# Optimization experiments

Hardware: AMD Instinct MI355X
Metric: run time of the kernel (lower is better)

Reference implementation:

```python
import jax, jax.numpy as jnp
import numpy as np

NUM_TASKS, IN_SIZE, OUT_SIZE, N_ROWS = 64, 512, 512, 2048


def setup_inputs() -> dict:
    key = jax.random.key(0)
    k_x, k_t, k_w = jax.random.split(key, 3)
    inputs = jax.random.normal(k_x, (N_ROWS, IN_SIZE), dtype=jnp.float32)
    task_ids = jax.random.randint(k_t, (N_ROWS,), 0, NUM_TASKS, dtype=jnp.int64)
    # in_size == out_size path: identity + N(0, 0.03) perturbation per task
    W = (jnp.eye(IN_SIZE, OUT_SIZE, dtype=jnp.float32)[None]
         + 0.03 * jax.random.normal(k_w, (NUM_TASKS, IN_SIZE, OUT_SIZE), dtype=jnp.float32))
    return {"inputs": inputs, "task_ids": task_ids, "W": W}


def reference(inputs, task_ids, W):
    # Gather the full per-row weight matrix then batched vector-matrix multiply,
    # faithful to torch.einsum('ni,nio->no', inputs, W[task_ids]).
    aligned = W[task_ids]                       # [I, in, out]
    return jnp.einsum("ni,nio->no", inputs, aligned)  # [I, out]
```

## Files before the change

kernel.cpp:

```cpp
#include <hip/hip_runtime.h>


#define NDIM 512
#define KDIM 512
#define NCOL 32
#define LISTCAP 256

typedef _Float16 f16x8 __attribute__((ext_vector_type(8)));
typedef float    f32x4 __attribute__((ext_vector_type(4)));
typedef int      i32x4 __attribute__((ext_vector_type(4)));

__global__ __launch_bounds__(256, 1) void k_wave(
    const float* __restrict__ x,
    const int*   __restrict__ tids,
    const float* __restrict__ W,
    float*       __restrict__ out,
    int n_rows)
{
    const int tid  = threadIdx.x;
    const int lane = tid & 63;
    const int wv   = tid >> 6;
    const int ml   = lane & 15;
    const int q    = lane >> 4;
    const int sc4  = (lane & 7) * 4;
    const int ol   = lane >> 3;

    const int bid   = blockIdx.x;
    const int task  = (bid & 7) | ((bid >> 5) << 3);
    const int chunk = ((bid >> 3) & 3) * 4 + wv;
    const int c0    = chunk * NCOL;

    __shared__ __align__(16) _Float16 Wt[4][NCOL * KDIM];
    __shared__ unsigned short rl[4][LISTCAP];

    _Float16*       Wm  = &Wt[wv][0];
    unsigned short* rlm = &rl[wv][0];

    const float* Wg = W + (size_t)task * KDIM * NDIM + c0;

    i32x4 tvv[8];
    #pragma unroll
    for (int cb = 0; cb < 8; ++cb) {
        const int r4 = cb * 256 + lane * 4;
        if (r4 + 3 < n_rows) {
            tvv[cb] = *(const i32x4*)(tids + r4);
        } else {
            #pragma unroll
            for (int j = 0; j < 4; ++j)
                tvv[cb][j] = (r4 + j < n_rows) ? tids[r4 + j] : -1;
        }
    }

    float4 wrA[8], wrB[8];
    auto issueS = [&](int s, float4 (&wb)[8]) {
        const size_t kb = (size_t)(ol + 8 * s) * 8;
        #pragma unroll
        for (int j = 0; j < 8; ++j)
            wb[j] = *(const float4*)(Wg + (kb + j) * NDIM + sc4);
    };
    auto stageS = [&](int s, const float4 (&wb)[8]) {
        const int oct = ol + 8 * s;
        #pragma unroll
        for (int j2 = 0; j2 < 4; ++j2) {
            f16x8 h8;
            #pragma unroll
            for (int j = 0; j < 8; ++j)
                h8[j] = (_Float16)(((const float*)&wb[j])[j2]);
            const int c  = sc4 + j2;
            const int po = oct ^ (c & 7);
            *(f16x8*)&Wm[c * KDIM + po * 8] = h8;
        }
    };

    issueS(0, wrA);
    issueS(1, wrB);

    int cnt = 0;
    #pragma unroll
    for (int cb = 0; cb < 8; ++cb) {
        #pragma unroll
        for (int j = 0; j < 4; ++j) {
            const bool m = (tvv[cb][j] == task);
            const unsigned long long bal = __ballot(m);
            const int rank = __popcll(bal & ((1ull << lane) - 1ull));
            const int slot = cnt + rank;
            if (m && slot < LISTCAP) rlm[slot] = (unsigned short)(cb * 256 + lane * 4 + j);
            cnt += __popcll(bal);
        }
    }
    if (cnt > LISTCAP) cnt = LISTCAP;

    stageS(0, wrA); issueS(2, wrA);
    stageS(1, wrB); issueS(3, wrB);
    stageS(2, wrA); issueS(4, wrA);
    stageS(3, wrB); issueS(5, wrB);
    stageS(4, wrA); issueS(6, wrA);
    stageS(5, wrB); issueS(7, wrB);
    stageS(6, wrA);
    stageS(7, wrB);

    f32x4 xqA[8], xqB[8];
    auto issueQ = [&](const float* xr, int qi, f32x4 (&xq)[8]) {
        #pragma unroll
        for (int s = 0; s < 4; ++s) {
            const int ks = qi * 4 + s;
            xq[2 * s]     = *(const f32x4*)(xr + ks * 32 + q * 8);
            xq[2 * s + 1] = *(const f32x4*)(xr + ks * 32 + q * 8 + 4);
        }
    };
    auto cvtQ = [&](const f32x4 (&xq)[8], f16x8* pf) {
        #pragma unroll
        for (int s = 0; s < 4; ++s) {
            f16x8 af;
            const float* a0 = (const float*)&xq[2 * s];
            #pragma unroll
            for (int j = 0; j < 8; ++j) af[j] = (_Float16)a0[j];
            pf[s] = af;
        }
    };
    auto mmaH = [&](int half, const f16x8* pf, f32x4& a0, f32x4& a1) {
        #pragma unroll
        for (int ksl = 0; ksl < 8; ++ksl) {
            const int oct = (half * 8 + ksl) * 4 + q;
            {
                const int po = oct ^ (ml & 7);
                const f16x8 bf = *(const f16x8*)&Wm[ml * KDIM + po * 8];
                a0 = __builtin_amdgcn_mfma_f32_16x16x32_f16(pf[ksl], bf, a0, 0, 0, 0);
            }
            {
                const int cB = 16 + ml;
                const int po = oct ^ (cB & 7);
                const f16x8 bf = *(const f16x8*)&Wm[cB * KDIM + po * 8];
                a1 = __builtin_amdgcn_mfma_f32_16x16x32_f16(pf[ksl], bf, a1, 0, 0, 0);
            }
        }
    };

    for (int g0 = 0; g0 < cnt; g0 += 16) {
        const int idx = g0 + ml;
        const int row = rlm[(idx < cnt) ? idx : (cnt - 1)];
        const float* xr = x + (size_t)row * KDIM;

        f16x8 pafA[8], pafB[8];
        f32x4 acc0 = {}, acc1 = {};

        issueQ(xr, 0, xqA);
        issueQ(xr, 1, xqB);
        cvtQ(xqA, pafA);     issueQ(xr, 2, xqA);
        cvtQ(xqB, pafA + 4); issueQ(xr, 3, xqB);
        mmaH(0, pafA, acc0, acc1);
        cvtQ(xqA, pafB);
        cvtQ(xqB, pafB + 4);
        mmaH(1, pafB, acc0, acc1);

        #pragma unroll
        for (int rg = 0; rg < 4; ++rg) {
            const int pos = g0 + q * 4 + rg;
            if (pos < cnt) {
                float* op = out + (size_t)rlm[pos] * NDIM + c0 + ml;
                op[0]  = acc0[rg];
                op[16] = acc1[rg];
            }
        }
    }
}

extern "C" void kernel_launch(void* const* d_in, const int* in_sizes, int n_in,
                              void* d_out, int out_size, void* d_ws, size_t ws_size,
                              hipStream_t stream) {
    const float* x    = (const float*)d_in[0];
    const int*   tids = (const int*)d_in[1];
    const float* W    = (const float*)d_in[2];
    float*       out  = (float*)d_out;
    const int n_rows  = in_sizes[1];

    k_wave<<<dim3(256), dim3(256), 0, stream>>>(x, tids, W, out, n_rows);
}
```

Baseline: 106.1 us.

## Split each wave's column chunk across four waves with 1024-thread blocks

Block size goes from 256 to 1024 threads, so four waves now share each 32-column chunk. Each wave stages a quarter of the chunk's weight tile into LDS, the block synchronises, and the waves then take interleaved 16-row groups of the matching row list. The aim is to cut per-wave serial weight staging and row-processing latency by raising wave-level parallelism per CU. The cost is a block-wide barrier, four waves each redoing the task-id ballot scan, and lower register headroom under launch bounds of 1024.

```diff
diff --git a/kernel.cpp b/kernel.cpp
--- a/kernel.cpp
+++ b/kernel.cpp
@@ -10,7 +10,7 @@
 typedef float    f32x4 __attribute__((ext_vector_type(4)));
 typedef int      i32x4 __attribute__((ext_vector_type(4)));
 
-__global__ __launch_bounds__(256, 1) void k_wave(
+__global__ __launch_bounds__(1024, 4) void k_big(
     const float* __restrict__ x,
     const int*   __restrict__ tids,
     const float* __restrict__ W,
@@ -25,16 +25,19 @@
     const int sc4  = (lane & 7) * 4;
     const int ol   = lane >> 3;
 
+    const int u    = wv >> 2;
+    const int sub  = wv & 3;
+
     const int bid   = blockIdx.x;
     const int task  = (bid & 7) | ((bid >> 5) << 3);
-    const int chunk = ((bid >> 3) & 3) * 4 + wv;
+    const int chunk = ((bid >> 3) & 3) * 4 + u;
     const int c0    = chunk * NCOL;
 
     __shared__ __align__(16) _Float16 Wt[4][NCOL * KDIM];
     __shared__ unsigned short rl[4][LISTCAP];
 
-    _Float16*       Wm  = &Wt[wv][0];
-    unsigned short* rlm = &rl[wv][0];
+    _Float16*       Wm  = &Wt[u][0];
+    unsigned short* rlm = &rl[u][0];
 
     const float* Wg = W + (size_t)task * KDIM * NDIM + c0;
 
@@ -51,29 +54,28 @@
         }
     }
 
-    float4 wrA[8], wrB[8];
-    auto issueS = [&](int s, float4 (&wb)[8]) {
+    float4 wr[8];
+    auto issueS = [&](int s) {
         const size_t kb = (size_t)(ol + 8 * s) * 8;
         #pragma unroll
         for (int j = 0; j < 8; ++j)
-            wb[j] = *(const float4*)(Wg + (kb + j) * NDIM + sc4);
+            wr[j] = *(const float4*)(Wg + (kb + j) * NDIM + sc4);
     };
-    auto stageS = [&](int s, const float4 (&wb)[8]) {
+    auto stageS = [&](int s) {
         const int oct = ol + 8 * s;
         #pragma unroll
         for (int j2 = 0; j2 < 4; ++j2) {
             f16x8 h8;
             #pragma unroll
             for (int j = 0; j < 8; ++j)
-                h8[j] = (_Float16)(((const float*)&wb[j])[j2]);
+                h8[j] = (_Float16)(((const float*)&wr[j])[j2]);
             const int c  = sc4 + j2;
             const int po = oct ^ (c & 7);
             *(f16x8*)&Wm[c * KDIM + po * 8] = h8;
         }
     };
 
-    issueS(0, wrA);
-    issueS(1, wrB);
+    issueS(2 * sub);
 
     int cnt = 0;
     #pragma unroll
@@ -90,14 +92,11 @@
     }
     if (cnt > LISTCAP) cnt = LISTCAP;
 
-    stageS(0, wrA); issueS(2, wrA);
-    stageS(1, wrB); issueS(3, wrB);
-    stageS(2, wrA); issueS(4, wrA);
-    stageS(3, wrB); issueS(5, wrB);
-    stageS(4, wrA); issueS(6, wrA);
-    stageS(5, wrB); issueS(7, wrB);
-    stageS(6, wrA);
-    stageS(7, wrB);
+    stageS(2 * sub);
+    issueS(2 * sub + 1);
+    stageS(2 * sub + 1);
+
+    __syncthreads();
 
     f32x4 xqA[8], xqB[8];
     auto issueQ = [&](const float* xr, int qi, f32x4 (&xq)[8]) {
@@ -136,7 +135,7 @@
         }
     };
 
-    for (int g0 = 0; g0 < cnt; g0 += 16) {
+    for (int g0 = sub * 16; g0 < cnt; g0 += 64) {
         const int idx = g0 + ml;
         const int row = rlm[(idx < cnt) ? idx : (cnt - 1)];
         const float* xr = x + (size_t)row * KDIM;
@@ -174,5 +173,5 @@
     float*       out  = (float*)d_out;
     const int n_rows  = in_sizes[1];
 
-    k_wave<<<dim3(256), dim3(256), 0, stream>>>(x, tids, W, out, n_rows);
+    k_big<<<dim3(256), dim3(1024), 0, stream>>>(x, tids, W, out, n_rows);
 }
```

New measurement: 126.2 us. 1.19x slower.
